# Kernel optimization log

Measured on AMD Instinct MI355X. Metric: run time of the kernel, lower is better.

## Reference

```python
import jax, jax.numpy as jnp
import numpy as np

NUM_HEADS = 12


def setup_inputs() -> dict:
    key = jax.random.key(0)
    ks = jax.random.split(key, 6)
    B, F, P, C = 2, 8, 196, 768
    N = 1 + F * P
    s = 0.02
    return {
        "x": jax.random.normal(ks[0], (B, N, C), jnp.float32),
        "Wqkv": jax.random.normal(ks[1], (C, 3 * C), jnp.float32) * s,
        "Wq": jax.random.normal(ks[2], (C, C), jnp.float32) * s,
        "Wkv": jax.random.normal(ks[3], (C, 2 * C), jnp.float32) * s,
        "Wproj": jax.random.normal(ks[4], (C, C), jnp.float32) * s,
        "bproj": jnp.zeros((C,), jnp.float32),
        "seq_len": 196,
        "num_frames": 8,
    }


def reference(x, Wqkv, Wq, Wkv, Wproj, bproj, seq_len, num_frames):
    B, N, C = x.shape
    H = NUM_HEADS
    d = C // H
    scale = d ** -0.5
    F, P = num_frames, seq_len
    S = F * P  # N == 1 + S

    qkv = x @ Wqkv                                # [B, N, 3C]
    q, k, v = jnp.split(qkv, 3, axis=-1)
    def to_heads(t):  # [B, N, C] -> [B*H, N, d]
        return t.reshape(B, N, H, d).transpose(0, 2, 1, 3).reshape(B * H, N, d)
    q, k, v = to_heads(q), to_heads(k), to_heads(v)

    # --- cls token attends over everything ---
    cls_q = q[:, :1] * scale                      # [BH, 1, d]
    cls_attn = jax.nn.softmax(jnp.einsum('bid,bjd->bij', cls_q, k), axis=-1)
    cls_out = jnp.einsum('bij,bjd->bid', cls_attn, v)  # [BH, 1, d]
    cls_out = cls_out.reshape(B, H, d).reshape(B, 1, C)

    # --- per-frame spatial softmax ---
    q_, k_, v_ = q[:, 1:], k[:, 1:], v[:, 1:]     # [BH, S, d]
    qk = jnp.einsum('bqd,bkd->bqk', q_, k_).reshape(B * H, S, F, P)
    sp_attn = jax.nn.softmax(scale * qk, axis=-1)  # softmax over patches within frame
    v_f = v_.reshape(B * H, F, P, d)
    xt = jnp.einsum('bqfn,bfnd->bqfd', sp_attn, v_f)  # [BH, S, F, d]

    x4 = xt.reshape(B, H, S, F, d).transpose(0, 2, 3, 1, 4).reshape(B, S, F, C)

    # --- diagonal extraction: query frame g == key frame f ---
    x5 = x4.reshape(B, F, P, F, C)
    xd = jnp.diagonal(x5, axis1=1, axis2=3)       # [B, P, C, F]
    xd = xd.transpose(0, 3, 1, 2).reshape(B, S, C)

    # --- temporal trajectory attention ---
    q2 = (xd @ Wq).reshape(B, S, H, d).transpose(0, 2, 1, 3) * scale  # [B,H,S,d]
    kv2 = x4 @ Wkv                                # [B, S, F, 2C]
    k2 = kv2[..., :C].reshape(B, S, F, H, d).transpose(0, 3, 1, 2, 4)  # [B,H,S,F,d]
    attn2 = jax.nn.softmax(jnp.einsum('bhsd,bhsfd->bhsf', q2, k2), axis=-1)
    # use_original_code=True: aggregate the trajectory tensor x4 itself
    xr = x4.reshape(B, S, F, H, d).transpose(0, 3, 1, 2, 4)            # [B,H,S,F,d]
    out = jnp.einsum('bhsf,bhsfd->bhsd', attn2, xr)
    out = out.transpose(0, 2, 1, 3).reshape(B, S, C)

    out = jnp.concatenate([cls_out, out], axis=1) @ Wproj + bproj      # [B, N, C]
    return out, attn2
```

## Files before the change

### kernel.cpp

```cpp
#include <hip/hip_runtime.h>

namespace {
constexpr int kB = 2;
constexpr int kH = 12;
constexpr int kD = 64;
constexpr int kC = 768;
constexpr int kF = 8;
constexpr int kP = 196;
constexpr int kS = kF * kP;
constexpr int kN = 1 + kS;
constexpr int k3C = 3 * kC;
constexpr float kScale = 0.125f;
constexpr int kBH = kB * kH;
constexpr int kPpad = 224;
constexpr int kPstr = 232;
constexpr int kLpad = 1600;
}

typedef __attribute__((ext_vector_type(8))) short bf16x8;
typedef __attribute__((ext_vector_type(4))) float f32x4;

__device__ inline ushort f2bf(float x) {
  union { float f; unsigned u; } v{x};
  unsigned r = v.u + 0x7fff + ((v.u >> 16) & 1);
  return (ushort)(r >> 16);
}
__device__ inline float bf2f(ushort u) {
  union { unsigned u; float f; } v{(unsigned)u << 16};
  return v.f;
}

__device__ __forceinline__ void gload_lds16(const void* g, void* l) {
  __builtin_amdgcn_global_load_lds(
      (const __attribute__((address_space(1))) unsigned int*)g,
      (__attribute__((address_space(3))) unsigned int*)l, 16, 0, 0);
}

__global__ __launch_bounds__(256) void gemm_bf16(
    const ushort* __restrict__ A, const ushort* __restrict__ Bt,
    const float* __restrict__ bias, float* __restrict__ C,
    int M, int N, int K, int nbx) {
  const int nwg = gridDim.x;
  const int q = nwg >> 3, rr = nwg & 7;
  const int xcd = blockIdx.x & 7, loc = blockIdx.x >> 3;
  const int vid = ((xcd < rr) ? xcd * (q + 1) : rr * (q + 1) + (xcd - rr) * q) + loc;
  const int m0 = (vid / nbx) * 128, n0 = (vid % nbx) * 128;

  __shared__ __align__(16) ushort As[128 * 32];
  __shared__ __align__(16) ushort Bs[128 * 32];
  const int tid = threadIdx.x;
  const int r0 = tid >> 2, c0 = tid & 3;
  const int r1 = r0 + 64;
  const int sc0 = (c0 ^ ((r0 >> 1) & 3)) * 8;
  const int sc1 = (c0 ^ ((r1 >> 1) & 3)) * 8;
  const int ar0 = min(m0 + r0, M - 1), ar1 = min(m0 + r1, M - 1);
  const ushort* ga0 = A + (size_t)ar0 * K + sc0;
  const ushort* ga1 = A + (size_t)ar1 * K + sc1;
  const ushort* gb0 = Bt + (size_t)(n0 + r0) * K + sc0;
  const ushort* gb1 = Bt + (size_t)(n0 + r1) * K + sc1;
  const int w = tid >> 6;
  char* lA0 = (char*)As + w * 1024;
  char* lA1 = (char*)As + 4096 + w * 1024;
  char* lB0 = (char*)Bs + w * 1024;
  char* lB1 = (char*)Bs + 4096 + w * 1024;
  const int lane = tid & 63;
  const int lr = lane & 15, lg = lane >> 4;
  const int wr = w >> 1, wc = w & 1;
  f32x4 acc[4][4] = {};
  for (int kt = 0; kt < K; kt += 32) {
    gload_lds16(ga0 + kt, lA0);
    gload_lds16(ga1 + kt, lA1);
    gload_lds16(gb0 + kt, lB0);
    gload_lds16(gb1 + kt, lB1);
    __syncthreads();
    bf16x8 af[4], bfr[4];
#pragma unroll
    for (int m = 0; m < 4; ++m) {
      int row = wr * 64 + m * 16 + lr;
      int ch = lg ^ ((row >> 1) & 3);
      af[m] = *(const bf16x8*)(As + row * 32 + ch * 8);
    }
#pragma unroll
    for (int n = 0; n < 4; ++n) {
      int row = wc * 64 + n * 16 + lr;
      int ch = lg ^ ((row >> 1) & 3);
      bfr[n] = *(const bf16x8*)(Bs + row * 32 + ch * 8);
    }
#pragma unroll
    for (int m = 0; m < 4; ++m)
#pragma unroll
      for (int n = 0; n < 4; ++n)
        acc[m][n] =
            __builtin_amdgcn_mfma_f32_16x16x32_bf16(af[m], bfr[n], acc[m][n], 0, 0, 0);
    __syncthreads();
  }
#pragma unroll
  for (int m = 0; m < 4; ++m) {
#pragma unroll
    for (int r = 0; r < 4; ++r) {
      const int mg = m0 + wr * 64 + m * 16 + lg * 4 + r;
      if (mg < M) {
        float* crow = C + (size_t)mg * N + n0 + wc * 64 + lr;
#pragma unroll
        for (int n = 0; n < 4; ++n) {
          float v = acc[m][n][r];
          if (bias) v += bias[n0 + wc * 64 + n * 16 + lr];
          crow[n * 16] = v;
        }
      }
    }
  }
}

__global__ void pack_x_k(const float* __restrict__ X, ushort* __restrict__ Xb,
                         int n4) {
  const int i = blockIdx.x * 256 + threadIdx.x;
  if (i >= n4) return;
  float4 v = ((const float4*)X)[i];
  ushort4 o = {f2bf(v.x), f2bf(v.y), f2bf(v.z), f2bf(v.w)};
  ((ushort4*)Xb)[i] = o;
}

__global__ __launch_bounds__(256) void pack_wt_k(const float* __restrict__ W,
                                                 ushort* __restrict__ Wt,
                                                 int ldw) {
  __shared__ float t[32][33];
  const int nb = blockIdx.x * 32;
  const int kb = blockIdx.y * 32;
  const int tx = threadIdx.x & 31, ty = threadIdx.x >> 5;
#pragma unroll
  for (int i = 0; i < 32; i += 8)
    t[ty + i][tx] = W[(size_t)(kb + ty + i) * ldw + nb + tx];
  __syncthreads();
#pragma unroll
  for (int i = 0; i < 32; i += 8)
    Wt[(size_t)(nb + ty + i) * 768 + kb + tx] = f2bf(t[tx][ty + i]);
}

__global__ void pack_qk_k(const float* __restrict__ qkv, ushort* __restrict__ Qb,
                          ushort* __restrict__ Kb) {
  const int idx = blockIdx.x * 256 + threadIdx.x;
  if (idx >= kBH * kS * kD) return;
  const int j = idx & 63;
  const int s = (idx >> 6) % kS;
  const int bh = idx / (kS * kD);
  const int b = bh / kH, h = bh % kH;
  const size_t src = (size_t)(b * kN + 1 + s) * k3C + h * kD + j;
  Qb[idx] = f2bf(qkv[src] * kScale);
  Kb[idx] = f2bf(qkv[src + kC]);
}

__global__ void pack_vt_k(const float* __restrict__ qkv, ushort* __restrict__ Vt) {
  const int idx = blockIdx.x * 256 + threadIdx.x;
  if (idx >= kBH * kF * kD * kPpad) return;
  const int n = idx % kPpad;
  const int j = (idx / kPpad) & 63;
  const int f = (idx / (kPpad * kD)) & 7;
  const int bh = idx / (kPpad * kD * kF);
  const int b = bh / kH, h = bh % kH;
  float v = 0.f;
  if (n < kP)
    v = qkv[(size_t)(b * kN + 1 + f * kP + n) * k3C + 2 * kC + h * kD + j];
  Vt[idx] = f2bf(v);
}

__global__ __launch_bounds__(128) void sp_attn_mfma(
    const ushort* __restrict__ Qb, const ushort* __restrict__ Kb,
    const ushort* __restrict__ Vt, ushort* __restrict__ x4b) {
  __shared__ __align__(16) ushort Pl[2][32 * kPstr];
  const int w = threadIdx.x >> 6;
  const int lane = threadIdx.x & 63;
  const int fbh = blockIdx.x;
  const int f = fbh / 24, bh = fbh % 24;
  const int tile = blockIdx.y * 2 + w;
  if (tile >= 49) return;
  const int q0 = tile * 32;
  const int lr = lane & 15;
  const int lg = lane >> 4;

  const ushort* qrow = Qb + ((size_t)bh * kS + q0 + lr) * kD + lg * 8;
  const bf16x8 a00 = *(const bf16x8*)qrow;
  const bf16x8 a01 = *(const bf16x8*)(qrow + 32);
  const bf16x8 a10 = *(const bf16x8*)(qrow + 16 * kD);
  const bf16x8 a11 = *(const bf16x8*)(qrow + 16 * kD + 32);

  f32x4 s0[13], s1[13];
  const ushort* kbase = Kb + ((size_t)bh * kS + f * kP + lr) * kD + lg * 8;
#pragma unroll
  for (int nt = 0; nt < 13; ++nt) {
    const ushort* kr = kbase + (size_t)nt * 16 * kD;
    bf16x8 b0 = *(const bf16x8*)kr;
    bf16x8 b1 = *(const bf16x8*)(kr + 32);
    f32x4 acc0 = {0.f, 0.f, 0.f, 0.f}, acc1 = {0.f, 0.f, 0.f, 0.f};
    acc0 = __builtin_amdgcn_mfma_f32_16x16x32_bf16(a00, b0, acc0, 0, 0, 0);
    acc0 = __builtin_amdgcn_mfma_f32_16x16x32_bf16(a01, b1, acc0, 0, 0, 0);
    acc1 = __builtin_amdgcn_mfma_f32_16x16x32_bf16(a10, b0, acc1, 0, 0, 0);
    acc1 = __builtin_amdgcn_mfma_f32_16x16x32_bf16(a11, b1, acc1, 0, 0, 0);
    s0[nt] = acc0;
    s1[nt] = acc1;
  }
  if (lr >= 4) {
#pragma unroll
    for (int r = 0; r < 4; ++r) { s0[12][r] = -1e30f; s1[12][r] = -1e30f; }
  }

  float inv0[4], inv1[4];
#pragma unroll
  for (int r = 0; r < 4; ++r) {
    float m = fmaxf(s0[0][r], s1[0][r]);
    float m0v = s0[0][r], m1v = s1[0][r];
#pragma unroll
    for (int nt = 1; nt < 13; ++nt) {
      m0v = fmaxf(m0v, s0[nt][r]);
      m1v = fmaxf(m1v, s1[nt][r]);
    }
#pragma unroll
    for (int o = 8; o; o >>= 1) {
      m0v = fmaxf(m0v, __shfl_xor(m0v, o, 16));
      m1v = fmaxf(m1v, __shfl_xor(m1v, o, 16));
    }
    float sum0 = 0.f, sum1 = 0.f;
    ushort* row0 = &Pl[w][(lg * 4 + r) * kPstr];
    ushort* row1 = &Pl[w][(16 + lg * 4 + r) * kPstr];
#pragma unroll
    for (int nt = 0; nt < 13; ++nt) {
      float p0 = __expf(s0[nt][r] - m0v);
      float p1 = __expf(s1[nt][r] - m1v);
      sum0 += p0;
      sum1 += p1;
      row0[nt * 16 + lr] = f2bf(p0);
      row1[nt * 16 + lr] = f2bf(p1);
    }
    row0[208 + lr] = 0;
    row1[208 + lr] = 0;
#pragma unroll
    for (int o = 8; o; o >>= 1) {
      sum0 += __shfl_xor(sum0, o, 16);
      sum1 += __shfl_xor(sum1, o, 16);
    }
    inv0[r] = 1.f / sum0;
    inv1[r] = 1.f / sum1;
  }

  const ushort* prow0 = &Pl[w][lr * kPstr + lg * 8];
  const ushort* prow1 = &Pl[w][(16 + lr) * kPstr + lg * 8];
  const ushort* vbase = Vt + ((size_t)(bh * kF + f) * kD + lr) * kPpad + lg * 8;
  f32x4 o0[4] = {}, o1[4] = {};
#pragma unroll
  for (int kt = 0; kt < 7; ++kt) {
    bf16x8 pa0 = *(const bf16x8*)(prow0 + kt * 32);
    bf16x8 pa1 = *(const bf16x8*)(prow1 + kt * 32);
#pragma unroll
    for (int nt2 = 0; nt2 < 4; ++nt2) {
      bf16x8 bv = *(const bf16x8*)(vbase + (size_t)nt2 * 16 * kPpad + kt * 32);
      o0[nt2] = __builtin_amdgcn_mfma_f32_16x16x32_bf16(pa0, bv, o0[nt2], 0, 0, 0);
      o1[nt2] = __builtin_amdgcn_mfma_f32_16x16x32_bf16(pa1, bv, o1[nt2], 0, 0, 0);
    }
  }

  const int b = bh / kH, h = bh % kH;
#pragma unroll
  for (int nt2 = 0; nt2 < 4; ++nt2) {
#pragma unroll
    for (int r = 0; r < 4; ++r) {
      const int srow0 = q0 + lg * 4 + r;
      x4b[(((size_t)(b * kS) + srow0) * kF + f) * kC + h * kD + nt2 * 16 + lr] =
          f2bf(o0[nt2][r] * inv0[r]);
      x4b[(((size_t)(b * kS) + srow0 + 16) * kF + f) * kC + h * kD + nt2 * 16 + lr] =
          f2bf(o1[nt2][r] * inv1[r]);
    }
  }
}

__global__ __launch_bounds__(256) void cls_logits_k(const float* __restrict__ qkv,
                                                    float* __restrict__ logits) {
  const int chunk = blockIdx.x, bh = blockIdx.y;
  const int b = bh / kH, h = bh % kH;
  const int g = threadIdx.x & 15, row = threadIdx.x >> 4;
  const size_t base = (size_t)b * kN * k3C;
  float4 q4 = *(const float4*)(qkv + base + h * kD + g * 4);
  q4.x *= kScale; q4.y *= kScale; q4.z *= kScale; q4.w *= kScale;
#pragma unroll
  for (int i = 0; i < 16; ++i) {
    const int n = chunk * 256 + i * 16 + row;
    if (n < kN) {
      const float4 kv =
          *(const float4*)(qkv + base + (size_t)n * k3C + kC + h * kD + g * 4);
      float p = q4.x * kv.x + q4.y * kv.y + q4.z * kv.z + q4.w * kv.w;
#pragma unroll
      for (int o = 8; o; o >>= 1) p += __shfl_xor(p, o, 16);
      if (g == 0) logits[bh * kLpad + n] = p;
    }
  }
}

__global__ __launch_bounds__(256) void cls_softmax_k(const float* __restrict__ logits,
                                                     float* __restrict__ pbuf) {
  __shared__ float red[8];
  const int bh = blockIdx.x, tid = threadIdx.x;
  float m = -1e30f;
  for (int n = tid; n < kN; n += 256) m = fmaxf(m, logits[bh * kLpad + n]);
#pragma unroll
  for (int o = 32; o; o >>= 1) m = fmaxf(m, __shfl_xor(m, o));
  if ((tid & 63) == 0) red[tid >> 6] = m;
  __syncthreads();
  m = fmaxf(fmaxf(red[0], red[1]), fmaxf(red[2], red[3]));
  float sum = 0.f;
  for (int n = tid; n < kN; n += 256) sum += __expf(logits[bh * kLpad + n] - m);
#pragma unroll
  for (int o = 32; o; o >>= 1) sum += __shfl_xor(sum, o);
  if ((tid & 63) == 0) red[4 + (tid >> 6)] = sum;
  __syncthreads();
  const float inv = 1.f / (red[4] + red[5] + red[6] + red[7]);
  for (int n = tid; n < kN; n += 256)
    pbuf[bh * kLpad + n] = __expf(logits[bh * kLpad + n] - m) * inv;
}

__global__ __launch_bounds__(256) void cls_pv_k(const float* __restrict__ qkv,
                                                const float* __restrict__ pbuf,
                                                float* __restrict__ partial) {
  __shared__ float pb[256];
  const int chunk = blockIdx.x, bh = blockIdx.y;
  const int b = bh / kH, h = bh % kH;
  const int j = threadIdx.x & 63, part = threadIdx.x >> 6;
  const size_t base = (size_t)b * kN * k3C + 2 * kC + h * kD + j;
  float acc = 0.f;
#pragma unroll 4
  for (int i = 0; i < 64; ++i) {
    const int n = chunk * 256 + i * 4 + part;
    if (n < kN) acc = fmaf(pbuf[bh * kLpad + n], qkv[base + (size_t)n * k3C], acc);
  }
  pb[threadIdx.x] = acc;
  __syncthreads();
  if (part == 0)
    partial[((size_t)bh * 7 + chunk) * kD + j] =
        pb[j] + pb[64 + j] + pb[128 + j] + pb[192 + j];
}

__global__ void cls_red_k(const float* __restrict__ partial,
                          ushort* __restrict__ xin_b) {
  const int bh = blockIdx.x, j = threadIdx.x;
  const int b = bh / kH, h = bh % kH;
  float s = 0.f;
#pragma unroll
  for (int c = 0; c < 7; ++c) s += partial[((size_t)bh * 7 + c) * kD + j];
  xin_b[(size_t)(b * kN) * kC + h * kD + j] = f2bf(s);
}

__global__ void xd_gather_k(const ushort* __restrict__ x4b,
                            ushort* __restrict__ xd_b) {
  const int idx = blockIdx.x * 256 + threadIdx.x;
  const int total = kB * kS * (kC / 8);
  if (idx >= total) return;
  const int row = idx / (kC / 8);
  const int cg = idx - row * (kC / 8);
  const int b = row / kS, s = row - b * kS;
  const int fq = s / kP;
  ((ulonglong2*)xd_b)[(size_t)row * (kC / 8) + cg] =
      ((const ulonglong2*)x4b)[((size_t)(b * kS + s) * kF + fq) * (kC / 8) + cg];
}

__global__ __launch_bounds__(256) void attn2_k(
    const float* __restrict__ q2, const float* __restrict__ k2,
    const ushort* __restrict__ x4b, ushort* __restrict__ xin_b,
    float* __restrict__ attn2out) {
  const int item = blockIdx.x * 4 + (threadIdx.x >> 6);
  const int lane = threadIdx.x & 63;
  const int s = item % kS;
  const int t = item / kS;
  const int h = t % kH, b = t / kH;
  const float qv = q2[(size_t)(b * kS + s) * kC + h * kD + lane] * kScale;
  float l[kF];
#pragma unroll
  for (int f = 0; f < kF; ++f) {
    float p = qv * k2[((size_t)(b * kS + s) * kF + f) * kC + h * kD + lane];
#pragma unroll
    for (int o = 32; o; o >>= 1) p += __shfl_xor(p, o);
    l[f] = p;
  }
  float m = l[0];
#pragma unroll
  for (int f = 1; f < kF; ++f) m = fmaxf(m, l[f]);
  float sum = 0.f;
#pragma unroll
  for (int f = 0; f < kF; ++f) {
    l[f] = __expf(l[f] - m);
    sum += l[f];
  }
  const float inv = 1.f / sum;
  float o = 0.f;
#pragma unroll
  for (int f = 0; f < kF; ++f)
    o = fmaf(l[f] * inv,
             bf2f(x4b[((size_t)(b * kS + s) * kF + f) * kC + h * kD + lane]), o);
  if (lane < kF)
    attn2out[((size_t)(b * kH + h) * kS + s) * kF + lane] = l[lane] * inv;
  xin_b[(size_t)(b * kN + 1 + s) * kC + h * kD + lane] = f2bf(o);
}

extern "C" void kernel_launch(void* const* d_in, const int* in_sizes, int n_in,
                              void* d_out, int out_size, void* d_ws,
                              size_t ws_size, hipStream_t stream) {
  const float* x = (const float*)d_in[0];
  const float* Wqkv = (const float*)d_in[1];
  const float* Wq = (const float*)d_in[2];
  const float* Wkv = (const float*)d_in[3];
  const float* Wproj = (const float*)d_in[4];
  const float* bproj = (const float*)d_in[5];

  char* p = (char*)d_ws;
  float* qkv = (float*)p;            p += (size_t)3138 * 2304 * 4;
  float* k2 = (float*)p;             p += (size_t)25088 * 768 * 4;
  float* q2 = (float*)p;             p += (size_t)3136 * 768 * 4;
  ushort* x4b = (ushort*)p;          p += (size_t)25088 * 768 * 2;
  ushort* xin_b = (ushort*)p;        p += (size_t)3138 * 768 * 2;
  ushort* xd_b = (ushort*)p;         p += (size_t)3136 * 768 * 2;
  ushort* xb = (ushort*)p;           p += (size_t)3138 * 768 * 2;
  ushort* Wqkv_t = (ushort*)p;       p += (size_t)2304 * 768 * 2;
  ushort* Wq_t = (ushort*)p;         p += (size_t)768 * 768 * 2;
  ushort* Wk_t = (ushort*)p;         p += (size_t)768 * 768 * 2;
  ushort* Wproj_t = (ushort*)p;      p += (size_t)768 * 768 * 2;
  ushort* Qb = (ushort*)p;           p += (size_t)kBH * kS * kD * 2;
  ushort* Kb = (ushort*)p;           p += ((size_t)kBH * kS + 16) * kD * 2;
  ushort* Vt = (ushort*)p;           p += (size_t)kBH * kF * kD * kPpad * 2;
  float* clsL = (float*)p;           p += (size_t)kBH * kLpad * 4;
  float* clsP = (float*)p;           p += (size_t)kBH * kLpad * 4;
  float* clsPart = (float*)p;

  float* out = (float*)d_out;
  float* attn2 = out + (size_t)kB * kN * kC;

  pack_x_k<<<(3138 * 768 / 4 + 255) / 256, 256, 0, stream>>>(x, xb, 3138 * 768 / 4);
  pack_wt_k<<<dim3(72, 24), 256, 0, stream>>>(Wqkv, Wqkv_t, 2304);
  pack_wt_k<<<dim3(24, 24), 256, 0, stream>>>(Wq, Wq_t, 768);
  pack_wt_k<<<dim3(24, 24), 256, 0, stream>>>(Wkv, Wk_t, 1536);
  pack_wt_k<<<dim3(24, 24), 256, 0, stream>>>(Wproj, Wproj_t, 768);
  gemm_bf16<<<18 * 25, 256, 0, stream>>>(xb, Wqkv_t, nullptr, qkv, 3138, 2304,
                                         768, 18);
  pack_qk_k<<<(kBH * kS * kD + 255) / 256, 256, 0, stream>>>(qkv, Qb, Kb);
  pack_vt_k<<<(kBH * kF * kD * kPpad + 255) / 256, 256, 0, stream>>>(qkv, Vt);
  cls_logits_k<<<dim3(7, 24), 256, 0, stream>>>(qkv, clsL);
  cls_softmax_k<<<24, 256, 0, stream>>>(clsL, clsP);
  cls_pv_k<<<dim3(7, 24), 256, 0, stream>>>(qkv, clsP, clsPart);
  cls_red_k<<<24, 64, 0, stream>>>(clsPart, xin_b);
  sp_attn_mfma<<<dim3(192, 25), 128, 0, stream>>>(Qb, Kb, Vt, x4b);
  xd_gather_k<<<(kB * kS * (kC / 8) + 255) / 256, 256, 0, stream>>>(x4b, xd_b);
  gemm_bf16<<<6 * 25, 256, 0, stream>>>(xd_b, Wq_t, nullptr, q2, 3136, 768,
                                        768, 6);
  gemm_bf16<<<6 * 196, 256, 0, stream>>>(x4b, Wk_t, nullptr, k2, 25088, 768,
                                         768, 6);
  attn2_k<<<9408, 256, 0, stream>>>(q2, k2, x4b, xin_b, attn2);
  gemm_bf16<<<6 * 25, 256, 0, stream>>>(xin_b, Wproj_t, bproj, out, 3138, 768,
                                        768, 6);
}
```

Measured before the change: 296.3 us.

## Keep softmax probs in registers and store k2/q2 intermediates in bf16

The spatial attention kernel now computes S transposed (K as the A operand), so each lane owns a query column. That lets the softmax reductions use two cross-group shuffles, and the P matrix is repacked into MFMA B-operand registers with lane shuffles instead of going through LDS. The block grows to 4 waves and the outputs are written as vectorized ushort4 stores. The templated GEMM now writes the q2 and k2 intermediates as bf16 instead of fp32, roughly halving the traffic of the large k2 tensor into attn2_k. The cost is lower precision on the temporal attention logits and more register pressure in the attention kernel.

```diff
diff --git a/kernel.cpp b/kernel.cpp
--- a/kernel.cpp
+++ b/kernel.cpp
@@ -13,12 +13,12 @@
 constexpr float kScale = 0.125f;
 constexpr int kBH = kB * kH;
 constexpr int kPpad = 224;
-constexpr int kPstr = 232;
 constexpr int kLpad = 1600;
 }
 
 typedef __attribute__((ext_vector_type(8))) short bf16x8;
 typedef __attribute__((ext_vector_type(4))) float f32x4;
+typedef __attribute__((ext_vector_type(4))) unsigned int u32x4;
 
 __device__ inline ushort f2bf(float x) {
   union { float f; unsigned u; } v{x};
@@ -36,9 +36,13 @@
       (__attribute__((address_space(3))) unsigned int*)l, 16, 0, 0);
 }
 
+__device__ inline void storeC(float v, float* p) { *p = v; }
+__device__ inline void storeC(float v, ushort* p) { *p = f2bf(v); }
+
+template <typename OutT>
 __global__ __launch_bounds__(256) void gemm_bf16(
     const ushort* __restrict__ A, const ushort* __restrict__ Bt,
-    const float* __restrict__ bias, float* __restrict__ C,
+    const float* __restrict__ bias, OutT* __restrict__ C,
     int M, int N, int K, int nbx) {
   const int nwg = gridDim.x;
   const int q = nwg >> 3, rr = nwg & 7;
@@ -100,12 +104,12 @@
     for (int r = 0; r < 4; ++r) {
       const int mg = m0 + wr * 64 + m * 16 + lg * 4 + r;
       if (mg < M) {
-        float* crow = C + (size_t)mg * N + n0 + wc * 64 + lr;
+        OutT* crow = C + (size_t)mg * N + n0 + wc * 64 + lr;
 #pragma unroll
         for (int n = 0; n < 4; ++n) {
           float v = acc[m][n][r];
           if (bias) v += bias[n0 + wc * 64 + n * 16 + lr];
-          crow[n * 16] = v;
+          storeC(v, crow + n * 16);
         }
       }
     }
@@ -164,15 +168,14 @@
   Vt[idx] = f2bf(v);
 }
 
-__global__ __launch_bounds__(128) void sp_attn_mfma(
+__global__ __launch_bounds__(256) void sp_attn_mfma(
     const ushort* __restrict__ Qb, const ushort* __restrict__ Kb,
     const ushort* __restrict__ Vt, ushort* __restrict__ x4b) {
-  __shared__ __align__(16) ushort Pl[2][32 * kPstr];
   const int w = threadIdx.x >> 6;
   const int lane = threadIdx.x & 63;
   const int fbh = blockIdx.x;
   const int f = fbh / 24, bh = fbh % 24;
-  const int tile = blockIdx.y * 2 + w;
+  const int tile = blockIdx.y * 4 + w;
   if (tile >= 49) return;
   const int q0 = tile * 32;
   const int lr = lane & 15;
@@ -192,83 +195,103 @@
     bf16x8 b0 = *(const bf16x8*)kr;
     bf16x8 b1 = *(const bf16x8*)(kr + 32);
     f32x4 acc0 = {0.f, 0.f, 0.f, 0.f}, acc1 = {0.f, 0.f, 0.f, 0.f};
-    acc0 = __builtin_amdgcn_mfma_f32_16x16x32_bf16(a00, b0, acc0, 0, 0, 0);
-    acc0 = __builtin_amdgcn_mfma_f32_16x16x32_bf16(a01, b1, acc0, 0, 0, 0);
-    acc1 = __builtin_amdgcn_mfma_f32_16x16x32_bf16(a10, b0, acc1, 0, 0, 0);
-    acc1 = __builtin_amdgcn_mfma_f32_16x16x32_bf16(a11, b1, acc1, 0, 0, 0);
+    acc0 = __builtin_amdgcn_mfma_f32_16x16x32_bf16(b0, a00, acc0, 0, 0, 0);
+    acc0 = __builtin_amdgcn_mfma_f32_16x16x32_bf16(b1, a01, acc0, 0, 0, 0);
+    acc1 = __builtin_amdgcn_mfma_f32_16x16x32_bf16(b0, a10, acc1, 0, 0, 0);
+    acc1 = __builtin_amdgcn_mfma_f32_16x16x32_bf16(b1, a11, acc1, 0, 0, 0);
     s0[nt] = acc0;
     s1[nt] = acc1;
   }
-  if (lr >= 4) {
+  if (lg >= 1) {
 #pragma unroll
     for (int r = 0; r < 4; ++r) { s0[12][r] = -1e30f; s1[12][r] = -1e30f; }
   }
 
-  float inv0[4], inv1[4];
-#pragma unroll
-  for (int r = 0; r < 4; ++r) {
-    float m = fmaxf(s0[0][r], s1[0][r]);
-    float m0v = s0[0][r], m1v = s1[0][r];
-#pragma unroll
-    for (int nt = 1; nt < 13; ++nt) {
-      m0v = fmaxf(m0v, s0[nt][r]);
-      m1v = fmaxf(m1v, s1[nt][r]);
-    }
-#pragma unroll
-    for (int o = 8; o; o >>= 1) {
-      m0v = fmaxf(m0v, __shfl_xor(m0v, o, 16));
-      m1v = fmaxf(m1v, __shfl_xor(m1v, o, 16));
-    }
-    float sum0 = 0.f, sum1 = 0.f;
-    ushort* row0 = &Pl[w][(lg * 4 + r) * kPstr];
-    ushort* row1 = &Pl[w][(16 + lg * 4 + r) * kPstr];
-#pragma unroll
-    for (int nt = 0; nt < 13; ++nt) {
-      float p0 = __expf(s0[nt][r] - m0v);
-      float p1 = __expf(s1[nt][r] - m1v);
-      sum0 += p0;
-      sum1 += p1;
-      row0[nt * 16 + lr] = f2bf(p0);
-      row1[nt * 16 + lr] = f2bf(p1);
-    }
-    row0[208 + lr] = 0;
-    row1[208 + lr] = 0;
-#pragma unroll
-    for (int o = 8; o; o >>= 1) {
-      sum0 += __shfl_xor(sum0, o, 16);
-      sum1 += __shfl_xor(sum1, o, 16);
-    }
-    inv0[r] = 1.f / sum0;
-    inv1[r] = 1.f / sum1;
-  }
-
-  const ushort* prow0 = &Pl[w][lr * kPstr + lg * 8];
-  const ushort* prow1 = &Pl[w][(16 + lr) * kPstr + lg * 8];
+  float m0 = -1e30f, m1 = -1e30f;
+#pragma unroll
+  for (int nt = 0; nt < 13; ++nt)
+#pragma unroll
+    for (int r = 0; r < 4; ++r) {
+      m0 = fmaxf(m0, s0[nt][r]);
+      m1 = fmaxf(m1, s1[nt][r]);
+    }
+  m0 = fmaxf(m0, __shfl_xor(m0, 16));
+  m0 = fmaxf(m0, __shfl_xor(m0, 32));
+  m1 = fmaxf(m1, __shfl_xor(m1, 16));
+  m1 = fmaxf(m1, __shfl_xor(m1, 32));
+
+  float sum0 = 0.f, sum1 = 0.f;
+  u32x4 breg0[7], breg1[7];
+#pragma unroll
+  for (int blk = 0; blk < 7; ++blk) {
+    unsigned pk0[2][2], pk1[2][2];
+#pragma unroll
+    for (int t = 0; t < 2; ++t) {
+      const int nt = blk * 2 + t;
+      if (nt < 13) {
+        float e0 = __expf(s0[nt][0] - m0), e1 = __expf(s0[nt][1] - m0);
+        float e2 = __expf(s0[nt][2] - m0), e3 = __expf(s0[nt][3] - m0);
+        sum0 += (e0 + e1) + (e2 + e3);
+        pk0[t][0] = ((unsigned)f2bf(e1) << 16) | f2bf(e0);
+        pk0[t][1] = ((unsigned)f2bf(e3) << 16) | f2bf(e2);
+        float g0 = __expf(s1[nt][0] - m1), g1 = __expf(s1[nt][1] - m1);
+        float g2 = __expf(s1[nt][2] - m1), g3 = __expf(s1[nt][3] - m1);
+        sum1 += (g0 + g1) + (g2 + g3);
+        pk1[t][0] = ((unsigned)f2bf(g1) << 16) | f2bf(g0);
+        pk1[t][1] = ((unsigned)f2bf(g3) << 16) | f2bf(g2);
+      } else {
+        pk0[t][0] = 0; pk0[t][1] = 0;
+        pk1[t][0] = 0; pk1[t][1] = 0;
+      }
+    }
+#pragma unroll
+    for (int j2 = 0; j2 < 4; ++j2) {
+      const int srcLane = ((lg & 1) * 2 + (j2 >> 1)) * 16 + lr;
+      unsigned t0 = (unsigned)__shfl((int)pk0[0][j2 & 1], srcLane);
+      unsigned t1 = (unsigned)__shfl((int)pk0[1][j2 & 1], srcLane);
+      breg0[blk][j2] = (lg < 2) ? t0 : t1;
+      unsigned u0 = (unsigned)__shfl((int)pk1[0][j2 & 1], srcLane);
+      unsigned u1 = (unsigned)__shfl((int)pk1[1][j2 & 1], srcLane);
+      breg1[blk][j2] = (lg < 2) ? u0 : u1;
+    }
+  }
+  sum0 += __shfl_xor(sum0, 16);
+  sum0 += __shfl_xor(sum0, 32);
+  sum1 += __shfl_xor(sum1, 16);
+  sum1 += __shfl_xor(sum1, 32);
+  const float inv0 = 1.f / sum0, inv1 = 1.f / sum1;
+
   const ushort* vbase = Vt + ((size_t)(bh * kF + f) * kD + lr) * kPpad + lg * 8;
   f32x4 o0[4] = {}, o1[4] = {};
 #pragma unroll
-  for (int kt = 0; kt < 7; ++kt) {
-    bf16x8 pa0 = *(const bf16x8*)(prow0 + kt * 32);
-    bf16x8 pa1 = *(const bf16x8*)(prow1 + kt * 32);
-#pragma unroll
-    for (int nt2 = 0; nt2 < 4; ++nt2) {
-      bf16x8 bv = *(const bf16x8*)(vbase + (size_t)nt2 * 16 * kPpad + kt * 32);
-      o0[nt2] = __builtin_amdgcn_mfma_f32_16x16x32_bf16(pa0, bv, o0[nt2], 0, 0, 0);
-      o1[nt2] = __builtin_amdgcn_mfma_f32_16x16x32_bf16(pa1, bv, o1[nt2], 0, 0, 0);
-    }
-  }
-
-  const int b = bh / kH, h = bh % kH;
-#pragma unroll
   for (int nt2 = 0; nt2 < 4; ++nt2) {
-#pragma unroll
-    for (int r = 0; r < 4; ++r) {
-      const int srow0 = q0 + lg * 4 + r;
-      x4b[(((size_t)(b * kS) + srow0) * kF + f) * kC + h * kD + nt2 * 16 + lr] =
-          f2bf(o0[nt2][r] * inv0[r]);
-      x4b[(((size_t)(b * kS) + srow0 + 16) * kF + f) * kC + h * kD + nt2 * 16 + lr] =
-          f2bf(o1[nt2][r] * inv1[r]);
-    }
+    const ushort* vb = vbase + (size_t)nt2 * 16 * kPpad;
+#pragma unroll
+    for (int blk = 0; blk < 7; ++blk) {
+      bf16x8 av = *(const bf16x8*)(vb + blk * 32);
+      bf16x8 pb0 = __builtin_bit_cast(bf16x8, breg0[blk]);
+      bf16x8 pb1 = __builtin_bit_cast(bf16x8, breg1[blk]);
+      o0[nt2] = __builtin_amdgcn_mfma_f32_16x16x32_bf16(av, pb0, o0[nt2], 0, 0, 0);
+      o1[nt2] = __builtin_amdgcn_mfma_f32_16x16x32_bf16(av, pb1, o1[nt2], 0, 0, 0);
+    }
+  }
+
+  const int b = bh / kH, h = bh % kH;
+  const size_t base0 =
+      ((size_t)(b * kS + q0 + lr) * kF + f) * kC + h * kD + lg * 4;
+#pragma unroll
+  for (int nt2 = 0; nt2 < 4; ++nt2) {
+    ushort4 v0, v1;
+    v0.x = f2bf(o0[nt2][0] * inv0);
+    v0.y = f2bf(o0[nt2][1] * inv0);
+    v0.z = f2bf(o0[nt2][2] * inv0);
+    v0.w = f2bf(o0[nt2][3] * inv0);
+    *(ushort4*)(x4b + base0 + nt2 * 16) = v0;
+    v1.x = f2bf(o1[nt2][0] * inv1);
+    v1.y = f2bf(o1[nt2][1] * inv1);
+    v1.z = f2bf(o1[nt2][2] * inv1);
+    v1.w = f2bf(o1[nt2][3] * inv1);
+    *(ushort4*)(x4b + base0 + (size_t)16 * kF * kC + nt2 * 16) = v1;
   }
 }
 
@@ -361,7 +384,7 @@
 }
 
 __global__ __launch_bounds__(256) void attn2_k(
-    const float* __restrict__ q2, const float* __restrict__ k2,
+    const ushort* __restrict__ q2b, const ushort* __restrict__ k2b,
     const ushort* __restrict__ x4b, ushort* __restrict__ xin_b,
     float* __restrict__ attn2out) {
   const int item = blockIdx.x * 4 + (threadIdx.x >> 6);
@@ -369,11 +392,11 @@
   const int s = item % kS;
   const int t = item / kS;
   const int h = t % kH, b = t / kH;
-  const float qv = q2[(size_t)(b * kS + s) * kC + h * kD + lane] * kScale;
+  const float qv = bf2f(q2b[(size_t)(b * kS + s) * kC + h * kD + lane]) * kScale;
   float l[kF];
 #pragma unroll
   for (int f = 0; f < kF; ++f) {
-    float p = qv * k2[((size_t)(b * kS + s) * kF + f) * kC + h * kD + lane];
+    float p = qv * bf2f(k2b[((size_t)(b * kS + s) * kF + f) * kC + h * kD + lane]);
 #pragma unroll
     for (int o = 32; o; o >>= 1) p += __shfl_xor(p, o);
     l[f] = p;
@@ -410,8 +433,8 @@
 
   char* p = (char*)d_ws;
   float* qkv = (float*)p;            p += (size_t)3138 * 2304 * 4;
-  float* k2 = (float*)p;             p += (size_t)25088 * 768 * 4;
-  float* q2 = (float*)p;             p += (size_t)3136 * 768 * 4;
+  ushort* k2b = (ushort*)p;          p += (size_t)25088 * 768 * 2;
+  ushort* q2b = (ushort*)p;          p += (size_t)3136 * 768 * 2;
   ushort* x4b = (ushort*)p;          p += (size_t)25088 * 768 * 2;
   ushort* xin_b = (ushort*)p;        p += (size_t)3138 * 768 * 2;
   ushort* xd_b = (ushort*)p;         p += (size_t)3136 * 768 * 2;
@@ -435,21 +458,21 @@
   pack_wt_k<<<dim3(24, 24), 256, 0, stream>>>(Wq, Wq_t, 768);
   pack_wt_k<<<dim3(24, 24), 256, 0, stream>>>(Wkv, Wk_t, 1536);
   pack_wt_k<<<dim3(24, 24), 256, 0, stream>>>(Wproj, Wproj_t, 768);
-  gemm_bf16<<<18 * 25, 256, 0, stream>>>(xb, Wqkv_t, nullptr, qkv, 3138, 2304,
-                                         768, 18);
+  gemm_bf16<float><<<18 * 25, 256, 0, stream>>>(xb, Wqkv_t, nullptr, qkv, 3138,
+                                                2304, 768, 18);
   pack_qk_k<<<(kBH * kS * kD + 255) / 256, 256, 0, stream>>>(qkv, Qb, Kb);
   pack_vt_k<<<(kBH * kF * kD * kPpad + 255) / 256, 256, 0, stream>>>(qkv, Vt);
   cls_logits_k<<<dim3(7, 24), 256, 0, stream>>>(qkv, clsL);
   cls_softmax_k<<<24, 256, 0, stream>>>(clsL, clsP);
   cls_pv_k<<<dim3(7, 24), 256, 0, stream>>>(qkv, clsP, clsPart);
   cls_red_k<<<24, 64, 0, stream>>>(clsPart, xin_b);
-  sp_attn_mfma<<<dim3(192, 25), 128, 0, stream>>>(Qb, Kb, Vt, x4b);
+  sp_attn_mfma<<<dim3(192, 13), 256, 0, stream>>>(Qb, Kb, Vt, x4b);
   xd_gather_k<<<(kB * kS * (kC / 8) + 255) / 256, 256, 0, stream>>>(x4b, xd_b);
-  gemm_bf16<<<6 * 25, 256, 0, stream>>>(xd_b, Wq_t, nullptr, q2, 3136, 768,
-                                        768, 6);
-  gemm_bf16<<<6 * 196, 256, 0, stream>>>(x4b, Wk_t, nullptr, k2, 25088, 768,
-                                         768, 6);
-  attn2_k<<<9408, 256, 0, stream>>>(q2, k2, x4b, xin_b, attn2);
-  gemm_bf16<<<6 * 25, 256, 0, stream>>>(xin_b, Wproj_t, bproj, out, 3138, 768,
-                                        768, 6);
-}
+  gemm_bf16<ushort><<<6 * 25, 256, 0, stream>>>(xd_b, Wq_t, nullptr, q2b, 3136,
+                                                768, 768, 6);
+  gemm_bf16<ushort><<<6 * 196, 256, 0, stream>>>(x4b, Wk_t, nullptr, k2b, 25088,
+                                                 768, 768, 6);
+  attn2_k<<<9408, 256, 0, stream>>>(q2b, k2b, x4b, xin_b, attn2);
+  gemm_bf16<float><<<6 * 25, 256, 0, stream>>>(xin_b, Wproj_t, bproj, out, 3138,
+                                               768, 768, 6);
+}
```

Result: faster. 281.6 us (-5.0%).
